# Optimization experiments

Measured on AMD Instinct MI355X. Metric: run time of the kernel, lower is better.

Reference implementation:

```python
import jax, jax.numpy as jnp
from jax import lax
import numpy as np

B, C, O, NF, H, W = 4, 64, 64, 64, 128, 128
DK = 3
K = DK * DK
PAD = DK // 2


def setup_inputs() -> dict:
    key = jax.random.key(0)
    k0, k1, k2, k3 = jax.random.split(key, 4)
    inputs = jax.random.normal(k0, (B, C, H, W), jnp.float32)
    feat = jax.random.normal(k1, (B, NF, H, W), jnp.float32)
    # small offset-conv weights keep learned offsets in a realistic sub-pixel range
    om_w = jax.random.normal(k2, (C * 3 * K, NF, 3, 3), jnp.float32) * 0.02
    om_b = jnp.zeros((C * 3 * K,), jnp.float32)
    dc_w = jax.random.normal(k3, (O, C, DK, DK), jnp.float32) * (1.0 / np.sqrt(C * K))
    dc_b = jnp.zeros((O,), jnp.float32)
    return dict(inputs=inputs, feat=feat, om_w=om_w, om_b=om_b, dc_w=dc_w, dc_b=dc_b)


def _gather(img, y, x):
    # img: [B,C,H,W]; y,x: int32 [B,C,K,H,W]; zero outside bounds
    valid = (y >= 0) & (y < H) & (x >= 0) & (x < W)
    yc = jnp.clip(y, 0, H - 1)
    xc = jnp.clip(x, 0, W - 1)
    idx = (yc * W + xc).reshape(B, C, K, H * W)
    flat = img.reshape(B, C, 1, H * W)
    v = jnp.take_along_axis(flat, idx, axis=3).reshape(B, C, K, H, W)
    return jnp.where(valid, v, 0.0)


def _forward(inputs, feat, om_w, om_b, dc_w, dc_b):
    # offset/mask conv: nf -> in_nc*3*K, 3x3, pad 1
    off_msk = lax.conv_general_dilated(
        feat, om_w, (1, 1), ((1, 1), (1, 1)),
        dimension_numbers=('NCHW', 'OIHW', 'NCHW')) + om_b[None, :, None, None]
    # offsets interleaved (y,x) per kernel tap per deformable group (= channel)
    off = off_msk[:, :C * 2 * K].reshape(B, C, K, 2, H, W)
    msk = jax.nn.sigmoid(off_msk[:, C * 2 * K:]).reshape(B, C, K, H, W)

    ky = (jnp.arange(K) // DK - PAD).astype(jnp.float32)  # [K]
    kx = (jnp.arange(K) % DK - PAD).astype(jnp.float32)
    hg = jnp.arange(H, dtype=jnp.float32)
    wg = jnp.arange(W, dtype=jnp.float32)
    py = hg[None, None, None, :, None] + ky[None, None, :, None, None] + off[:, :, :, 0]  # [B,C,K,H,W]
    px = wg[None, None, None, None, :] + kx[None, None, :, None, None] + off[:, :, :, 1]

    y0f = jnp.floor(py); x0f = jnp.floor(px)
    wy = py - y0f; wx = px - x0f
    y0 = y0f.astype(jnp.int32); x0 = x0f.astype(jnp.int32)
    y1 = y0 + 1; x1 = x0 + 1

    v00 = _gather(inputs, y0, x0)
    v01 = _gather(inputs, y0, x1)
    v10 = _gather(inputs, y1, x0)
    v11 = _gather(inputs, y1, x1)
    sampled = ((1 - wy) * (1 - wx) * v00 + (1 - wy) * wx * v01
               + wy * (1 - wx) * v10 + wy * wx * v11) * msk  # [B,C,K,H,W]

    out = jnp.einsum('bckhw,ock->bohw', sampled, dc_w.reshape(O, C, K))
    out = out + dc_b[None, :, None, None]
    return jax.nn.relu(out)


def reference(inputs, feat, om_w, om_b, dc_w, dc_b):
    return _forward(inputs, feat, om_w, om_b, dc_w, dc_b)
```

## Files before the change

kernel.cpp:

```cpp
#include <hip/hip_runtime.h>
#include <hip/hip_bf16.h>

typedef __bf16 bf16;
typedef __bf16 bf16x8 __attribute__((ext_vector_type(8)));
typedef __bf16 bf16x4 __attribute__((ext_vector_type(4)));
typedef float f32x4 __attribute__((ext_vector_type(4)));

#define MFMA16(a, b, c) __builtin_amdgcn_mfma_f32_16x16x32_bf16((a), (b), (c), 0, 0, 0)

static constexpr size_t FEAT_OFF = 0;
static constexpr size_t OMW_OFF  = 8388608;
static constexpr size_t OMB_OFF  = OMW_OFF + 1990656;
static constexpr size_t DCW_OFF  = OMB_OFF + 6912;

__global__ void prep_cvt(const float* __restrict__ in, bf16* __restrict__ out, int n) {
    int i = blockIdx.x * 256 + threadIdx.x;
    if (i < n) out[i] = (bf16)in[i];
}

__global__ void prep_w(const float* __restrict__ om_w, const float* __restrict__ om_b,
                       bf16* __restrict__ om_w_r, float* __restrict__ om_b_r) {
    int i = blockIdx.x * 256 + threadIdx.x;
    if (i < 1728 * 576) {
        int m = i / 576, k = i - m * 576;
        int t = m / 576, ck = m - t * 576;
        int ch = (t < 2) ? (ck * 2 + t) : (1152 + ck);
        int tap = k >> 6, cf = k & 63;
        om_w_r[i] = (bf16)om_w[ch * 576 + cf * 9 + tap];
    }
    if (i < 1728) {
        int t = i / 576, ck = i - t * 576;
        int ch = (t < 2) ? (ck * 2 + t) : (1152 + ck);
        om_b_r[i] = om_b[ch];
    }
}


__global__ void __launch_bounds__(256, 2)
deform_fused(const float* __restrict__ inputs,
             const bf16* __restrict__ featbf,
             const bf16* __restrict__ omwr,
             const float* __restrict__ ombr,
             const bf16* __restrict__ dcbf,
             const float* __restrict__ dcb,
             float* __restrict__ out)
{
    const int bh = blockIdx.x;
    const int b = bh >> 7, h = bh & 127;
    const int tid = threadIdx.x;
    const int lane = tid & 63, wid = tid >> 6;
    const int l15 = lane & 15, g = lane >> 4;

    __shared__ __align__(16) unsigned char smem[49920 + 8192];
    char* featB = (char*)smem;
    char* sampB = (char*)smem + 49920;

    for (int i = tid; i < 12480; i += 256) ((unsigned*)featB)[i] = 0u;
    __syncthreads();
    if (tid < 192) {
        const int ky = tid >> 6, cf = tid & 63;
        const int hh = h - 1 + ky;
        if ((unsigned)hh < 128u) {
            const bf16* src = featbf + (size_t)((b * 64 + cf) * 128 + hh) * 128;
            const int cfb = cf >> 3, cfl = (cf & 7) << 1;
            for (int c0 = 0; c0 < 128; c0 += 8) {
                bf16x8 v = *(const bf16x8*)(src + c0);
#pragma unroll
                for (int e = 0; e < 8; ++e) {
                    int pc = c0 + e + 1;
                    *(bf16*)(featB + (ky * 130 + pc) * 128 + ((cfb ^ (pc & 7)) << 4) + cfl) = v[e];
                }
            }
        }
    }
    __syncthreads();

    f32x4 acc2[8];
#pragma unroll
    for (int nf = 0; nf < 8; ++nf) acc2[nf] = (f32x4){0.f, 0.f, 0.f, 0.f};

    const bf16* dcrow = dcbf + (size_t)(wid * 16 + l15) * 576;

    for (int blk = 0; blk < 9; ++blk) {
        f32x4 acc1[3][8];
#pragma unroll
        for (int t = 0; t < 3; ++t)
#pragma unroll
            for (int nf = 0; nf < 8; ++nf) acc1[t][nf] = (f32x4){0.f, 0.f, 0.f, 0.f};

        const int arow = blk * 64 + wid * 16 + l15;
        const bf16* ar0 = omwr + (size_t)arow * 576;
        const bf16* ar1 = omwr + (size_t)(576 + arow) * 576;
        const bf16* ar2 = omwr + (size_t)(1152 + arow) * 576;

#pragma unroll 2
        for (int kk = 0; kk < 18; ++kk) {
            const int koff = kk * 32 + g * 8;
            bf16x8 a0 = *(const bf16x8*)(ar0 + koff);
            bf16x8 a1 = *(const bf16x8*)(ar1 + koff);
            bf16x8 a2 = *(const bf16x8*)(ar2 + koff);
            const int tap = kk >> 1;
            const int kyp = tap / 3, kxp = tap - 3 * kyp;
            const int base = (kyp * 130 + kxp + l15) * 128
                           + ((((kk & 1) * 4 + g) ^ ((l15 + kxp) & 7)) << 4);
#pragma unroll
            for (int nf = 0; nf < 8; ++nf) {
                bf16x8 bfr = *(const bf16x8*)(featB + base + nf * 2048);
                acc1[0][nf] = MFMA16(a0, bfr, acc1[0][nf]);
                acc1[1][nf] = MFMA16(a1, bfr, acc1[1][nf]);
                acc1[2][nf] = MFMA16(a2, bfr, acc1[2][nf]);
            }
        }

        int cpl[4], dyv[4], dxv[4];
        float by[4], bx[4], bm[4];
#pragma unroll
        for (int r = 0; r < 4; ++r) {
            int ck = blk * 64 + wid * 16 + g * 4 + r;
            int c = ck / 9, kd = ck - 9 * c, kq = kd / 3;
            cpl[r] = c; dyv[r] = kq - 1; dxv[r] = kd - 3 * kq - 1;
            by[r] = ombr[ck]; bx[r] = ombr[576 + ck]; bm[r] = ombr[1152 + ck];
        }

        bf16x8 aK0 = *(const bf16x8*)(dcrow + blk * 64 + g * 8);
        bf16x8 aK1 = *(const bf16x8*)(dcrow + blk * 64 + 32 + g * 8);

#pragma unroll
        for (int half = 0; half < 2; ++half) {
#pragma unroll
            for (int u = 0; u < 4; ++u) {
                const int nf = half * 4 + u;
                float s[4];
#pragma unroll
                for (int r = 0; r < 4; ++r) {
                    float offy = acc1[0][nf][r] + by[r];
                    float offx = acc1[1][nf][r] + bx[r];
                    float lg   = acc1[2][nf][r] + bm[r];
                    float py = (float)(h + dyv[r]) + offy;
                    float px = (float)(nf * 16 + l15 + dxv[r]) + offx;
                    float y0f = floorf(py), x0f = floorf(px);
                    float wy = py - y0f, wx = px - x0f;
                    int y0 = (int)y0f, x0 = (int)x0f;
                    int y1 = y0 + 1, x1 = x0 + 1;
                    const float* pl = inputs + ((size_t)(b * 64 + cpl[r]) << 14);
                    int y0c = min(max(y0, 0), 127), y1c = min(max(y1, 0), 127);
                    int x0c = min(max(x0, 0), 127), x1c = min(max(x1, 0), 127);
                    bool vy0 = (unsigned)y0 < 128u, vy1 = (unsigned)y1 < 128u;
                    bool vx0 = (unsigned)x0 < 128u, vx1 = (unsigned)x1 < 128u;
                    float v00 = (vy0 && vx0) ? pl[(y0c << 7) + x0c] : 0.f;
                    float v01 = (vy0 && vx1) ? pl[(y0c << 7) + x1c] : 0.f;
                    float v10 = (vy1 && vx0) ? pl[(y1c << 7) + x0c] : 0.f;
                    float v11 = (vy1 && vx1) ? pl[(y1c << 7) + x1c] : 0.f;
                    float bil = (1.f - wy) * ((1.f - wx) * v00 + wx * v01)
                              + wy * ((1.f - wx) * v10 + wx * v11);
                    float msk = __builtin_amdgcn_rcpf(1.f + __expf(-lg));
                    s[r] = bil * msk;
                }
                bf16x4 p = {(bf16)s[0], (bf16)s[1], (bf16)s[2], (bf16)s[3]};
                *(bf16x4*)(sampB + (u * 16 + l15) * 128
                           + (((wid * 4 + g) ^ ((l15 & 7) << 1)) << 3)) = p;
            }
            __syncthreads();
#pragma unroll
            for (int u = 0; u < 4; ++u) {
                const int nf = half * 4 + u;
                const int rb = (u * 16 + l15) * 128;
                bf16x8 b0 = *(const bf16x8*)(sampB + rb + ((g ^ (l15 & 7)) << 4));
                bf16x8 b1 = *(const bf16x8*)(sampB + rb + (((4 + g) ^ (l15 & 7)) << 4));
                acc2[nf] = MFMA16(aK0, b0, acc2[nf]);
                acc2[nf] = MFMA16(aK1, b1, acc2[nf]);
            }
            __syncthreads();
        }
    }

    float bias[4];
#pragma unroll
    for (int r = 0; r < 4; ++r) bias[r] = dcb[wid * 16 + g * 4 + r];
#pragma unroll
    for (int nf = 0; nf < 8; ++nf)
#pragma unroll
        for (int r = 0; r < 4; ++r) {
            int o = wid * 16 + g * 4 + r;
            out[(size_t)((b * 64 + o) * 128 + h) * 128 + nf * 16 + l15]
                = fmaxf(acc2[nf][r] + bias[r], 0.f);
        }
}

extern "C" void kernel_launch(void* const* d_in, const int* in_sizes, int n_in,
                              void* d_out, int out_size, void* d_ws, size_t ws_size,
                              hipStream_t stream) {
    const float* inputs = (const float*)d_in[0];
    const float* feat   = (const float*)d_in[1];
    const float* om_w   = (const float*)d_in[2];
    const float* om_b   = (const float*)d_in[3];
    const float* dc_w   = (const float*)d_in[4];
    const float* dc_b   = (const float*)d_in[5];
    float* out = (float*)d_out;

    char* ws = (char*)d_ws;
    bf16*  featbf = (bf16*)(ws + FEAT_OFF);
    bf16*  omwr   = (bf16*)(ws + OMW_OFF);
    float* ombr   = (float*)(ws + OMB_OFF);
    bf16*  dcbf   = (bf16*)(ws + DCW_OFF);

    prep_cvt<<<(4194304 + 255) / 256, 256, 0, stream>>>(feat, featbf, 4194304);
    prep_w<<<(995328 + 255) / 256, 256, 0, stream>>>(om_w, om_b, omwr, ombr);
    prep_cvt<<<(36864 + 255) / 256, 256, 0, stream>>>(dc_w, dcbf, 36864);

    deform_fused<<<512, 256, 0, stream>>>(inputs, featbf, omwr, ombr, dcbf, dc_b, out);
}
```

Before: 219.6 us.

## Split waves over channel and pixel halves, feed MFMA from registers, drop sample LDS

Warps now split into two channel-tap halves and two pixel halves, each computing 32 offset rows by 64 pixels instead of 16 rows by 128 pixels. The sampled values are packed straight into registers as the B operand of the second MFMA, which removes the LDS staging buffer and the per-half barriers. The price is a cross-wave reduction through LDS at the end. Weights are pre-swizzled into a lane-contiguous MFMA fragment layout so that A-operand loads are coalesced. This trades more register use and a final reduction for fewer barriers and better weight-load patterns.

Result: slower. 499.1 us (+127.3%).

```diff
diff --git a/kernel.cpp b/kernel.cpp
--- a/kernel.cpp
+++ b/kernel.cpp
@@ -9,29 +9,43 @@
 #define MFMA16(a, b, c) __builtin_amdgcn_mfma_f32_16x16x32_bf16((a), (b), (c), 0, 0, 0)
 
 static constexpr size_t FEAT_OFF = 0;
-static constexpr size_t OMW_OFF  = 8388608;
-static constexpr size_t OMB_OFF  = OMW_OFF + 1990656;
-static constexpr size_t DCW_OFF  = OMB_OFF + 6912;
+static constexpr size_t OMW3_OFF = 8388608;
+static constexpr size_t OMB_OFF  = OMW3_OFF + 1990656;
+static constexpr size_t DCW2_OFF = OMB_OFF + 6912;
 
 __global__ void prep_cvt(const float* __restrict__ in, bf16* __restrict__ out, int n) {
     int i = blockIdx.x * 256 + threadIdx.x;
     if (i < n) out[i] = (bf16)in[i];
 }
 
-__global__ void prep_w(const float* __restrict__ om_w, const float* __restrict__ om_b,
-                       bf16* __restrict__ om_w_r, float* __restrict__ om_b_r) {
+__global__ void prep_omw3(const float* __restrict__ om_w, bf16* __restrict__ out) {
     int i = blockIdx.x * 256 + threadIdx.x;
-    if (i < 1728 * 576) {
-        int m = i / 576, k = i - m * 576;
-        int t = m / 576, ck = m - t * 576;
-        int ch = (t < 2) ? (ck * 2 + t) : (1152 + ck);
-        int tap = k >> 6, cf = k & 63;
-        om_w_r[i] = (bf16)om_w[ch * 576 + cf * 9 + tap];
+    if (i >= 995328) return;
+    int e = i & 511, lane = e >> 3, j = e & 7;
+    int q = i >> 9;
+    int t = q % 3, q2 = q / 3, kk = q2 % 18, ct = q2 / 18;
+    int ck = ct * 16 + (lane & 15);
+    int kcol = kk * 32 + (lane >> 4) * 8 + j;
+    int tap = kcol >> 6, cf = kcol & 63;
+    int ch = (t < 2) ? (ck * 2 + t) : (1152 + ck);
+    out[i] = (bf16)om_w[ch * 576 + cf * 9 + tap];
+}
+
+__global__ void prep_dcw2(const float* __restrict__ dc_w, const float* __restrict__ om_b,
+                          bf16* __restrict__ dcw2, float* __restrict__ ombr) {
+    int i = blockIdx.x * 256 + threadIdx.x;
+    if (i < 36864) {
+        int e = i & 511, lane = e >> 3, j = e & 7;
+        int q = i >> 9;
+        int ot = q & 3, win = q >> 2;
+        int o = ot * 16 + (lane & 15), gg = lane >> 4;
+        int ck = win * 32 + ((j < 4) ? (gg * 4 + j) : (16 + gg * 4 + (j - 4)));
+        dcw2[i] = (bf16)dc_w[o * 576 + ck];
     }
     if (i < 1728) {
         int t = i / 576, ck = i - t * 576;
         int ch = (t < 2) ? (ck * 2 + t) : (1152 + ck);
-        om_b_r[i] = om_b[ch];
+        ombr[i] = om_b[ch];
     }
 }
 
@@ -39,9 +53,9 @@
 __global__ void __launch_bounds__(256, 2)
 deform_fused(const float* __restrict__ inputs,
              const bf16* __restrict__ featbf,
-             const bf16* __restrict__ omwr,
+             const bf16* __restrict__ omw3,
              const float* __restrict__ ombr,
-             const bf16* __restrict__ dcbf,
+             const bf16* __restrict__ dcw2,
              const float* __restrict__ dcb,
              float* __restrict__ out)
 {
@@ -50,12 +64,11 @@
     const int tid = threadIdx.x;
     const int lane = tid & 63, wid = tid >> 6;
     const int l15 = lane & 15, g = lane >> 4;
-
-    __shared__ __align__(16) unsigned char smem[49920 + 8192];
-    char* featB = (char*)smem;
-    char* sampB = (char*)smem + 49920;
-
-    for (int i = tid; i < 12480; i += 256) ((unsigned*)featB)[i] = 0u;
+    const int ckh = wid & 1, pxh = wid >> 1;
+
+    __shared__ __align__(16) unsigned char smem[49920];
+
+    for (int i = tid; i < 12480; i += 256) ((unsigned*)smem)[i] = 0u;
     __syncthreads();
     if (tid < 192) {
         const int ky = tid >> 6, cf = tid & 63;
@@ -68,76 +81,82 @@
 #pragma unroll
                 for (int e = 0; e < 8; ++e) {
                     int pc = c0 + e + 1;
-                    *(bf16*)(featB + (ky * 130 + pc) * 128 + ((cfb ^ (pc & 7)) << 4) + cfl) = v[e];
+                    *(bf16*)(smem + (ky * 130 + pc) * 128 + ((cfb ^ (pc & 7)) << 4) + cfl) = v[e];
                 }
             }
         }
     }
     __syncthreads();
 
-    f32x4 acc2[8];
-#pragma unroll
-    for (int nf = 0; nf < 8; ++nf) acc2[nf] = (f32x4){0.f, 0.f, 0.f, 0.f};
-
-    const bf16* dcrow = dcbf + (size_t)(wid * 16 + l15) * 576;
+    f32x4 acc2[4][4];
+#pragma unroll
+    for (int ot = 0; ot < 4; ++ot)
+#pragma unroll
+        for (int nf = 0; nf < 4; ++nf) acc2[ot][nf] = (f32x4){0.f, 0.f, 0.f, 0.f};
 
     for (int blk = 0; blk < 9; ++blk) {
-        f32x4 acc1[3][8];
+        f32x4 acc1[3][2][4];
 #pragma unroll
         for (int t = 0; t < 3; ++t)
 #pragma unroll
-            for (int nf = 0; nf < 8; ++nf) acc1[t][nf] = (f32x4){0.f, 0.f, 0.f, 0.f};
-
-        const int arow = blk * 64 + wid * 16 + l15;
-        const bf16* ar0 = omwr + (size_t)arow * 576;
-        const bf16* ar1 = omwr + (size_t)(576 + arow) * 576;
-        const bf16* ar2 = omwr + (size_t)(1152 + arow) * 576;
+            for (int ct = 0; ct < 2; ++ct)
+#pragma unroll
+                for (int nf = 0; nf < 4; ++nf) acc1[t][ct][nf] = (f32x4){0.f, 0.f, 0.f, 0.f};
+
+        const int ct0 = blk * 4 + ckh * 2;
 
 #pragma unroll 2
         for (int kk = 0; kk < 18; ++kk) {
-            const int koff = kk * 32 + g * 8;
-            bf16x8 a0 = *(const bf16x8*)(ar0 + koff);
-            bf16x8 a1 = *(const bf16x8*)(ar1 + koff);
-            bf16x8 a2 = *(const bf16x8*)(ar2 + koff);
             const int tap = kk >> 1;
             const int kyp = tap / 3, kxp = tap - 3 * kyp;
-            const int base = (kyp * 130 + kxp + l15) * 128
-                           + ((((kk & 1) * 4 + g) ^ ((l15 + kxp) & 7)) << 4);
-#pragma unroll
-            for (int nf = 0; nf < 8; ++nf) {
-                bf16x8 bfr = *(const bf16x8*)(featB + base + nf * 2048);
-                acc1[0][nf] = MFMA16(a0, bfr, acc1[0][nf]);
-                acc1[1][nf] = MFMA16(a1, bfr, acc1[1][nf]);
-                acc1[2][nf] = MFMA16(a2, bfr, acc1[2][nf]);
-            }
-        }
-
-        int cpl[4], dyv[4], dxv[4];
-        float by[4], bx[4], bm[4];
-#pragma unroll
-        for (int r = 0; r < 4; ++r) {
-            int ck = blk * 64 + wid * 16 + g * 4 + r;
-            int c = ck / 9, kd = ck - 9 * c, kq = kd / 3;
-            cpl[r] = c; dyv[r] = kq - 1; dxv[r] = kd - 3 * kq - 1;
-            by[r] = ombr[ck]; bx[r] = ombr[576 + ck]; bm[r] = ombr[1152 + ck];
-        }
-
-        bf16x8 aK0 = *(const bf16x8*)(dcrow + blk * 64 + g * 8);
-        bf16x8 aK1 = *(const bf16x8*)(dcrow + blk * 64 + 32 + g * 8);
-
-#pragma unroll
-        for (int half = 0; half < 2; ++half) {
-#pragma unroll
-            for (int u = 0; u < 4; ++u) {
-                const int nf = half * 4 + u;
+            bf16x8 a[2][3];
+#pragma unroll
+            for (int ct = 0; ct < 2; ++ct)
+#pragma unroll
+                for (int t = 0; t < 3; ++t)
+                    a[ct][t] = *(const bf16x8*)(omw3
+                        + (size_t)((((ct0 + ct) * 18 + kk) * 3 + t) * 512) + lane * 8);
+            const int pcb = pxh * 64 + l15 + kxp;
+            const int base = (kyp * 130 + pcb) * 128 + ((((kk & 1) * 4 + g) ^ (pcb & 7)) << 4);
+#pragma unroll
+            for (int nf = 0; nf < 4; ++nf) {
+                bf16x8 bfr = *(const bf16x8*)(smem + base + nf * 2048);
+#pragma unroll
+                for (int ct = 0; ct < 2; ++ct) {
+                    acc1[0][ct][nf] = MFMA16(a[ct][0], bfr, acc1[0][ct][nf]);
+                    acc1[1][ct][nf] = MFMA16(a[ct][1], bfr, acc1[1][ct][nf]);
+                    acc1[2][ct][nf] = MFMA16(a[ct][2], bfr, acc1[2][ct][nf]);
+                }
+            }
+        }
+
+        bf16x8 aK[4];
+#pragma unroll
+        for (int ot = 0; ot < 4; ++ot)
+            aK[ot] = *(const bf16x8*)(dcw2 + (size_t)(((blk * 2 + ckh) * 4 + ot) * 512) + lane * 8);
+
+        bf16x4 p[2][4];
+#pragma unroll
+        for (int ct = 0; ct < 2; ++ct) {
+            int cpl[4], dyv[4], dxv[4];
+            float by[4], bx[4], bm[4];
+#pragma unroll
+            for (int r = 0; r < 4; ++r) {
+                int ck = blk * 64 + ckh * 32 + ct * 16 + g * 4 + r;
+                int c = ck / 9, kd = ck - 9 * c, kq = kd / 3;
+                cpl[r] = c; dyv[r] = kq - 1; dxv[r] = kd - 3 * kq - 1;
+                by[r] = ombr[ck]; bx[r] = ombr[576 + ck]; bm[r] = ombr[1152 + ck];
+            }
+#pragma unroll
+            for (int nf = 0; nf < 4; ++nf) {
                 float s[4];
 #pragma unroll
                 for (int r = 0; r < 4; ++r) {
-                    float offy = acc1[0][nf][r] + by[r];
-                    float offx = acc1[1][nf][r] + bx[r];
-                    float lg   = acc1[2][nf][r] + bm[r];
+                    float offy = acc1[0][ct][nf][r] + by[r];
+                    float offx = acc1[1][ct][nf][r] + bx[r];
+                    float lg   = acc1[2][ct][nf][r] + bm[r];
                     float py = (float)(h + dyv[r]) + offy;
-                    float px = (float)(nf * 16 + l15 + dxv[r]) + offx;
+                    float px = (float)(pxh * 64 + nf * 16 + l15 + dxv[r]) + offx;
                     float y0f = floorf(py), x0f = floorf(px);
                     float wy = py - y0f, wx = px - x0f;
                     int y0 = (int)y0f, x0 = (int)x0f;
@@ -156,35 +175,46 @@
                     float msk = __builtin_amdgcn_rcpf(1.f + __expf(-lg));
                     s[r] = bil * msk;
                 }
-                bf16x4 p = {(bf16)s[0], (bf16)s[1], (bf16)s[2], (bf16)s[3]};
-                *(bf16x4*)(sampB + (u * 16 + l15) * 128
-                           + (((wid * 4 + g) ^ ((l15 & 7) << 1)) << 3)) = p;
-            }
-            __syncthreads();
-#pragma unroll
-            for (int u = 0; u < 4; ++u) {
-                const int nf = half * 4 + u;
-                const int rb = (u * 16 + l15) * 128;
-                bf16x8 b0 = *(const bf16x8*)(sampB + rb + ((g ^ (l15 & 7)) << 4));
-                bf16x8 b1 = *(const bf16x8*)(sampB + rb + (((4 + g) ^ (l15 & 7)) << 4));
-                acc2[nf] = MFMA16(aK0, b0, acc2[nf]);
-                acc2[nf] = MFMA16(aK1, b1, acc2[nf]);
-            }
-            __syncthreads();
-        }
-    }
-
-    float bias[4];
-#pragma unroll
-    for (int r = 0; r < 4; ++r) bias[r] = dcb[wid * 16 + g * 4 + r];
-#pragma unroll
-    for (int nf = 0; nf < 8; ++nf)
-#pragma unroll
-        for (int r = 0; r < 4; ++r) {
-            int o = wid * 16 + g * 4 + r;
-            out[(size_t)((b * 64 + o) * 128 + h) * 128 + nf * 16 + l15]
-                = fmaxf(acc2[nf][r] + bias[r], 0.f);
-        }
+                p[ct][nf] = (bf16x4){(bf16)s[0], (bf16)s[1], (bf16)s[2], (bf16)s[3]};
+            }
+        }
+
+#pragma unroll
+        for (int nf = 0; nf < 4; ++nf) {
+            bf16x8 bfr = __builtin_shufflevector(p[0][nf], p[1][nf], 0, 1, 2, 3, 4, 5, 6, 7);
+#pragma unroll
+            for (int ot = 0; ot < 4; ++ot)
+                acc2[ot][nf] = MFMA16(aK[ot], bfr, acc2[ot][nf]);
+        }
+    }
+
+    __syncthreads();
+    float* red = (float*)smem;
+    if (ckh == 0) {
+#pragma unroll
+        for (int ot = 0; ot < 4; ++ot)
+#pragma unroll
+            for (int nf = 0; nf < 4; ++nf)
+#pragma unroll
+                for (int r = 0; r < 4; ++r)
+                    red[pxh * 4352 + (ot * 16 + g * 4 + r) * 68 + nf * 16 + l15] = acc2[ot][nf][r];
+    }
+    __syncthreads();
+    if (ckh == 1) {
+#pragma unroll
+        for (int ot = 0; ot < 4; ++ot)
+#pragma unroll
+            for (int nf = 0; nf < 4; ++nf)
+#pragma unroll
+                for (int r = 0; r < 4; ++r)
+                    red[pxh * 4352 + (ot * 16 + g * 4 + r) * 68 + nf * 16 + l15] += acc2[ot][nf][r];
+    }
+    __syncthreads();
+    for (int i = tid; i < 8192; i += 256) {
+        int pair = i >> 12, rem = i & 4095, o = rem >> 6, pxl = rem & 63;
+        float v = red[pair * 4352 + o * 68 + pxl] + dcb[o];
+        out[((size_t)(b * 64 + o) * 128 + h) * 128 + pair * 64 + pxl] = fmaxf(v, 0.f);
+    }
 }
 
 extern "C" void kernel_launch(void* const* d_in, const int* in_sizes, int n_in,
@@ -200,13 +230,13 @@
 
     char* ws = (char*)d_ws;
     bf16*  featbf = (bf16*)(ws + FEAT_OFF);
-    bf16*  omwr   = (bf16*)(ws + OMW_OFF);
+    bf16*  omw3   = (bf16*)(ws + OMW3_OFF);
     float* ombr   = (float*)(ws + OMB_OFF);
-    bf16*  dcbf   = (bf16*)(ws + DCW_OFF);
+    bf16*  dcw2   = (bf16*)(ws + DCW2_OFF);
 
     prep_cvt<<<(4194304 + 255) / 256, 256, 0, stream>>>(feat, featbf, 4194304);
-    prep_w<<<(995328 + 255) / 256, 256, 0, stream>>>(om_w, om_b, omwr, ombr);
-    prep_cvt<<<(36864 + 255) / 256, 256, 0, stream>>>(dc_w, dcbf, 36864);
-
-    deform_fused<<<512, 256, 0, stream>>>(inputs, featbf, omwr, ombr, dcbf, dc_b, out);
-}
+    prep_omw3<<<(995328 + 255) / 256, 256, 0, stream>>>(om_w, omw3);
+    prep_dcw2<<<(36864 + 255) / 256, 256, 0, stream>>>(dc_w, om_b, dcw2, ombr);
+
+    deform_fused<<<512, 256, 0, stream>>>(inputs, featbf, omw3, ombr, dcw2, dc_b, out);
+}
```
